# Optimization experiments

Measured on AMD Instinct MI355X. Metric: run time of the kernel, lower is better.

The kernel has to match this reference:

```python
import jax, jax.numpy as jnp
import numpy as np

B, S, D = 2, 2048, 2048
H = 16
HD = D // H
FF = 8192
EPS = 1e-5


def _layer_norm(x, g, b):
    mu = jnp.mean(x, axis=-1, keepdims=True)
    var = jnp.mean(jnp.square(x - mu), axis=-1, keepdims=True)
    return (x - mu) * jax.lax.rsqrt(var + EPS) * g + b


def setup_inputs() -> dict:
    key = jax.random.key(0)
    ks = jax.random.split(key, 8)
    s = 0.02
    return {
        "x": jax.random.normal(ks[0], (B, S, D), dtype=jnp.float32),
        "ln1_g": jnp.ones((D,), jnp.float32),
        "ln1_b": jnp.zeros((D,), jnp.float32),
        "qkv_w": jax.random.normal(ks[1], (D, 3 * D), dtype=jnp.float32) * s,
        "qkv_b": jnp.zeros((3 * D,), jnp.float32),
        "out_w": jax.random.normal(ks[2], (D, D), dtype=jnp.float32) * s,
        "out_b": jnp.zeros((D,), jnp.float32),
        "ln2_g": jnp.ones((D,), jnp.float32),
        "ln2_b": jnp.zeros((D,), jnp.float32),
        "w1": jax.random.normal(ks[3], (D, FF), dtype=jnp.float32) * s,
        "b1": jnp.zeros((FF,), jnp.float32),
        "w2": jax.random.normal(ks[4], (FF, D), dtype=jnp.float32) * s,
        "b2": jnp.zeros((D,), jnp.float32),
    }


def reference(x, ln1_g, ln1_b, qkv_w, qkv_b, out_w, out_b, ln2_g, ln2_b, w1, b1, w2, b2):
    # --- attention sub-block (pre-norm) ---
    residual = x
    h = _layer_norm(x, ln1_g, ln1_b)
    qkv = h @ qkv_w + qkv_b                      # [B,S,3D]
    q, k, v = jnp.split(qkv, 3, axis=-1)
    # [B,S,D] -> [B,H,S,HD]
    q = q.reshape(B, S, H, HD).transpose(0, 2, 1, 3)
    k = k.reshape(B, S, H, HD).transpose(0, 2, 1, 3)
    v = v.reshape(B, S, H, HD).transpose(0, 2, 1, 3)
    scores = jnp.einsum("bhqd,bhkd->bhqk", q, k)  # [B,H,S,S]
    causal = jnp.triu(jnp.ones((S, S), dtype=bool), k=1)
    scores = jnp.where(causal[None, None], -jnp.inf, scores)
    attn = jax.nn.softmax(scores / np.sqrt(HD).astype(np.float32), axis=-1)
    av = jnp.einsum("bhqk,bhkd->bhqd", attn, v)   # [B,H,S,HD]
    av = av.transpose(0, 2, 1, 3).reshape(B, S, D)
    x = residual + (av @ out_w + out_b)
    # --- FFN sub-block (pre-norm) ---
    residual = x
    h = _layer_norm(x, ln2_g, ln2_b)
    h = jax.nn.gelu(h @ w1 + b1, approximate=False)
    x = residual + (h @ w2 + b2)
    return x
```

## Files before the change

### kernel.cpp

```cpp
#include <hip/hip_runtime.h>
#include <hip/hip_bf16.h>

#define B_  2
#define S_  2048
#define D_  2048
#define H_  16
#define HD_ 128
#define FF_ 8192

typedef __bf16 bf16x8 __attribute__((ext_vector_type(8)));
typedef float  f32x4  __attribute__((ext_vector_type(4)));
typedef unsigned short u16;
typedef u16 u16x8 __attribute__((ext_vector_type(8)));

__device__ __forceinline__ u16 f2bf(float f) {
    union { float f; unsigned u; } c; c.f = f;
    unsigned u = c.u;
    u += 0x7fffu + ((u >> 16) & 1u);
    return (u16)(u >> 16);
}

__device__ __forceinline__ void gld16(void* lds, const void* g) {
    __builtin_amdgcn_global_load_lds(
        (const __attribute__((address_space(1))) unsigned int*)g,
        (__attribute__((address_space(3))) unsigned int*)lds,
        16, 0, 0);
}

__global__ __launch_bounds__(256)
void ln_kernel(const float* __restrict__ x, const float* __restrict__ g,
               const float* __restrict__ bb, u16* __restrict__ out)
{
    int row = blockIdx.x, tid = threadIdx.x;
    const float4* xr = (const float4*)(x + (size_t)row * D_);
    float4 a = xr[tid], c = xr[tid + 256];
    float s  = a.x + a.y + a.z + a.w + c.x + c.y + c.z + c.w;
    float s2 = a.x*a.x + a.y*a.y + a.z*a.z + a.w*a.w
             + c.x*c.x + c.y*c.y + c.z*c.z + c.w*c.w;
    #pragma unroll
    for (int off = 32; off > 0; off >>= 1) {
        s  += __shfl_down(s,  off, 64);
        s2 += __shfl_down(s2, off, 64);
    }
    __shared__ float red[16];
    __shared__ float mr[2];
    int wid = tid >> 6, lane = tid & 63;
    if (lane == 0) { red[wid] = s; red[8 + wid] = s2; }
    __syncthreads();
    if (tid == 0) {
        float ts = red[0] + red[1] + red[2] + red[3];
        float t2 = red[8] + red[9] + red[10] + red[11];
        float mu = ts * (1.0f / D_);
        float var = t2 * (1.0f / D_) - mu * mu;
        mr[0] = mu; mr[1] = rsqrtf(var + 1e-5f);
    }
    __syncthreads();
    float mu = mr[0], rstd = mr[1];
    const float4* gg = (const float4*)g;
    const float4* bv = (const float4*)bb;
    float4 g0 = gg[tid], g1 = gg[tid + 256];
    float4 b0 = bv[tid], b1 = bv[tid + 256];
    u16* orow = out + (size_t)row * D_;
    ushort4 o0, o1;
    o0.x = f2bf((a.x - mu) * rstd * g0.x + b0.x);
    o0.y = f2bf((a.y - mu) * rstd * g0.y + b0.y);
    o0.z = f2bf((a.z - mu) * rstd * g0.z + b0.z);
    o0.w = f2bf((a.w - mu) * rstd * g0.w + b0.w);
    o1.x = f2bf((c.x - mu) * rstd * g1.x + b1.x);
    o1.y = f2bf((c.y - mu) * rstd * g1.y + b1.y);
    o1.z = f2bf((c.z - mu) * rstd * g1.z + b1.z);
    o1.w = f2bf((c.w - mu) * rstd * g1.w + b1.w);
    *(ushort4*)&orow[tid * 4]         = o0;
    *(ushort4*)&orow[(tid + 256) * 4] = o1;
}

__global__ __launch_bounds__(256)
void tcvt_kernel(const float* __restrict__ W, u16* __restrict__ WT, int K, int N)
{
    __shared__ float t[32][33];
    int n0 = blockIdx.x << 5, k0 = blockIdx.y << 5;
    int tx = threadIdx.x & 31, ty = threadIdx.x >> 5;
    #pragma unroll
    for (int i = 0; i < 32; i += 8)
        t[ty + i][tx] = W[(size_t)(k0 + ty + i) * N + n0 + tx];
    __syncthreads();
    #pragma unroll
    for (int i = 0; i < 32; i += 8)
        WT[(size_t)(n0 + ty + i) * K + k0 + tx] = f2bf(t[tx][ty + i]);
}

template<int EPI>
__global__ __launch_bounds__(256)
void gemm_kernel(const u16* __restrict__ A, const u16* __restrict__ BT,
                 const float* __restrict__ bias, const float* __restrict__ res,
                 void* __restrict__ outv, int M, int N, int K)
{
    __shared__ u16 ldsA[128 * 32];
    __shared__ u16 ldsB[128 * 32];
    int tid = threadIdx.x;
    int wid = tid >> 6, lane = tid & 63;
    int wm = wid >> 1, wn = wid & 1;
    int quad = lane >> 4, l16 = lane & 15;
    int m0 = blockIdx.y << 7, n0 = blockIdx.x << 7;

    f32x4 acc[4][4] = {};

    const u16* gA0 = A  + (size_t)(m0 + wid * 32 + (lane >> 2)) * K + ((lane & 3) << 3);
    const u16* gA1 = gA0 + (size_t)16 * K;
    const u16* gB0 = BT + (size_t)(n0 + wid * 32 + (lane >> 2)) * K + ((lane & 3) << 3);
    const u16* gB1 = gB0 + (size_t)16 * K;
    u16* lA0 = ldsA + wid * 1024;
    u16* lA1 = ldsA + wid * 1024 + 512;
    u16* lB0 = ldsB + wid * 1024;
    u16* lB1 = ldsB + wid * 1024 + 512;

    for (int k0 = 0; k0 < K; k0 += 32) {
        gld16(lA0, gA0 + k0);
        gld16(lA1, gA1 + k0);
        gld16(lB0, gB0 + k0);
        gld16(lB1, gB1 + k0);
        __syncthreads();
        bf16x8 af[4], bf[4];
        #pragma unroll
        for (int t = 0; t < 4; t++) {
            af[t] = *(const bf16x8*)&ldsA[(wm * 64 + t * 16 + l16) * 32 + quad * 8];
            bf[t] = *(const bf16x8*)&ldsB[(wn * 64 + t * 16 + l16) * 32 + quad * 8];
        }
        #pragma unroll
        for (int i = 0; i < 4; i++)
            #pragma unroll
            for (int j = 0; j < 4; j++)
                acc[i][j] = __builtin_amdgcn_mfma_f32_16x16x32_bf16(af[i], bf[j], acc[i][j], 0, 0, 0);
        __syncthreads();
    }

    u16*   outb = (u16*)outv;
    float* outf = (float*)outv;
    int colb = n0 + wn * 64, rowb = m0 + wm * 64;
    #pragma unroll
    for (int j = 0; j < 4; j++) {
        int col = colb + j * 16 + l16;
        float bv = bias[col];
        #pragma unroll
        for (int i = 0; i < 4; i++) {
            int row0 = rowb + i * 16 + (quad << 2);
            #pragma unroll
            for (int r = 0; r < 4; r++) {
                float v = acc[i][j][r] + bv;
                size_t idx = (size_t)(row0 + r) * N + col;
                if (EPI == 2) {
                    outf[idx] = v + res[idx];
                } else {
                    if (EPI == 1) v = 0.5f * v * (1.0f + erff(v * 0.70710678118654752f));
                    outb[idx] = f2bf(v);
                }
            }
        }
    }
}

__global__ __launch_bounds__(256, 2)
void attn_kernel(const u16* __restrict__ qkv, u16* __restrict__ av)
{
    __shared__ u16 ldsK[4][64][32];
    __shared__ unsigned ldsVT[128][36];
    __shared__ u16 ldsP[4][32][72];
    int tid = threadIdx.x, wid = tid >> 6, lane = tid & 63;
    int quad = lane >> 4, l16 = lane & 15;
    int bh = blockIdx.y, b = bh >> 4, h = bh & 15;
    int qx = gridDim.x - 1 - blockIdx.x;
    int q0 = qx << 7;
    const u16* base = qkv + (size_t)b * S_ * (3 * D_);

    bf16x8 aq[2][4];
    #pragma unroll
    for (int set = 0; set < 2; set++) {
        int qrow = q0 + set * 64 + wid * 16 + l16;
        const u16* qp = base + (size_t)qrow * (3 * D_) + h * HD_;
        #pragma unroll
        for (int kk = 0; kk < 4; kk++)
            aq[set][kk] = *(const bf16x8*)(qp + kk * 32 + quad * 8);
    }

    float m_i[2][4], l_i[2][4];
    f32x4 oacc[2][8] = {};
    #pragma unroll
    for (int s = 0; s < 2; s++)
        #pragma unroll
        for (int r = 0; r < 4; r++) { m_i[s][r] = -1e30f; l_i[s][r] = 0.f; }

    const float scale = 0.088388347648318447f;
    int ntile = 2 * qx + 2;
    for (int jt = 0; jt < ntile; jt++) {
        int j0 = jt << 6;
        #pragma unroll
        for (int j = 0; j < 4; j++) {
            int c = wid * 4 + j;
            int kk = c >> 2, kb = c & 3;
            int key = (kb << 4) + (lane >> 2);
            const u16* g = base + (size_t)(j0 + key) * (3 * D_) + D_ + h * HD_
                         + kk * 32 + ((lane & 3) << 3);
            gld16((u16*)ldsK + c * 512, g);
        }
        {
            int kp = lane & 31, dhalf = lane >> 5;
            #pragma unroll
            for (int p = 0; p < 2; p++) {
                int doff = wid * 32 + p * 16 + dhalf * 8;
                const u16* g0 = base + (size_t)(j0 + 2 * kp) * (3 * D_)
                              + 2 * D_ + h * HD_ + doff;
                u16x8 v0 = *(const u16x8*)g0;
                u16x8 v1 = *(const u16x8*)(g0 + 3 * D_);
                #pragma unroll
                for (int k = 0; k < 8; k++)
                    ldsVT[doff + k][kp] = (unsigned)v0[k] | ((unsigned)v1[k] << 16);
            }
        }
        __syncthreads();
        f32x4 sacc[2][4] = {};
        #pragma unroll
        for (int kk = 0; kk < 4; kk++)
            #pragma unroll
            for (int n = 0; n < 4; n++) {
                bf16x8 bfr = *(const bf16x8*)&ldsK[kk][(n << 4) + l16][quad << 3];
                sacc[0][n] = __builtin_amdgcn_mfma_f32_16x16x32_bf16(aq[0][kk], bfr, sacc[0][n], 0, 0, 0);
                sacc[1][n] = __builtin_amdgcn_mfma_f32_16x16x32_bf16(aq[1][kk], bfr, sacc[1][n], 0, 0, 0);
            }
        #pragma unroll
        for (int set = 0; set < 2; set++) {
            float rowmax[4] = {-1e30f, -1e30f, -1e30f, -1e30f};
            #pragma unroll
            for (int n = 0; n < 4; n++) {
                int key = j0 + (n << 4) + l16;
                #pragma unroll
                for (int r = 0; r < 4; r++) {
                    float xv = sacc[set][n][r] * scale;
                    int qr = q0 + set * 64 + wid * 16 + (quad << 2) + r;
                    if (key > qr) xv = -1e30f;
                    sacc[set][n][r] = xv;
                    rowmax[r] = fmaxf(rowmax[r], xv);
                }
            }
            #pragma unroll
            for (int off = 1; off < 16; off <<= 1)
                #pragma unroll
                for (int r = 0; r < 4; r++)
                    rowmax[r] = fmaxf(rowmax[r], __shfl_xor(rowmax[r], off, 64));
            float alpha[4], rsum[4];
            #pragma unroll
            for (int r = 0; r < 4; r++) {
                float mn = fmaxf(m_i[set][r], rowmax[r]);
                alpha[r] = __expf(m_i[set][r] - mn);
                m_i[set][r] = mn;
                rsum[r] = 0.f;
            }
            #pragma unroll
            for (int n = 0; n < 4; n++)
                #pragma unroll
                for (int r = 0; r < 4; r++) {
                    float p = __expf(sacc[set][n][r] - m_i[set][r]);
                    rsum[r] += p;
                    ldsP[wid][set * 16 + (quad << 2) + r][(n << 4) + l16] = f2bf(p);
                }
            #pragma unroll
            for (int off = 1; off < 16; off <<= 1)
                #pragma unroll
                for (int r = 0; r < 4; r++)
                    rsum[r] += __shfl_xor(rsum[r], off, 64);
            #pragma unroll
            for (int r = 0; r < 4; r++)
                l_i[set][r] = l_i[set][r] * alpha[r] + rsum[r];
            #pragma unroll
            for (int n = 0; n < 8; n++)
                #pragma unroll
                for (int r = 0; r < 4; r++)
                    oacc[set][n][r] *= alpha[r];
        }
        #pragma unroll
        for (int ks = 0; ks < 2; ks++) {
            bf16x8 pa0 = *(const bf16x8*)&ldsP[wid][l16]     [(ks << 5) + (quad << 3)];
            bf16x8 pa1 = *(const bf16x8*)&ldsP[wid][16 + l16][(ks << 5) + (quad << 3)];
            #pragma unroll
            for (int n = 0; n < 8; n++) {
                bf16x8 vb = *(const bf16x8*)&ldsVT[(n << 4) + l16][(ks << 4) + (quad << 2)];
                oacc[0][n] = __builtin_amdgcn_mfma_f32_16x16x32_bf16(pa0, vb, oacc[0][n], 0, 0, 0);
                oacc[1][n] = __builtin_amdgcn_mfma_f32_16x16x32_bf16(pa1, vb, oacc[1][n], 0, 0, 0);
            }
        }
        __syncthreads();
    }
    #pragma unroll
    for (int set = 0; set < 2; set++)
        #pragma unroll
        for (int r = 0; r < 4; r++) {
            float inv = 1.0f / l_i[set][r];
            int qr = q0 + set * 64 + wid * 16 + (quad << 2) + r;
            u16* op = av + (size_t)(b * S_ + qr) * D_ + h * HD_;
            #pragma unroll
            for (int n = 0; n < 8; n++)
                op[(n << 4) + l16] = f2bf(oacc[set][n][r] * inv);
        }
}

extern "C" void kernel_launch(void* const* d_in, const int* in_sizes, int n_in,
                              void* d_out, int out_size, void* d_ws, size_t ws_size,
                              hipStream_t stream)
{
    const float* x     = (const float*)d_in[0];
    const float* ln1_g = (const float*)d_in[1];
    const float* ln1_b = (const float*)d_in[2];
    const float* qkv_w = (const float*)d_in[3];
    const float* qkv_b = (const float*)d_in[4];
    const float* out_w = (const float*)d_in[5];
    const float* out_b = (const float*)d_in[6];
    const float* ln2_g = (const float*)d_in[7];
    const float* ln2_b = (const float*)d_in[8];
    const float* w1    = (const float*)d_in[9];
    const float* b1    = (const float*)d_in[10];
    const float* w2    = (const float*)d_in[11];
    const float* b2    = (const float*)d_in[12];
    float* out = (float*)d_out;

    char* ws  = (char*)d_ws;
    u16* wT   = (u16*)ws;
    u16* hbuf = (u16*)(ws + (32u << 20));
    u16* big  = (u16*)(ws + (48u << 20));
    u16* qkvb = big;
    u16* ffb  = big;

    dim3 blk(256);

    ln_kernel<<<dim3(B_ * S_), blk, 0, stream>>>(x, ln1_g, ln1_b, hbuf);
    tcvt_kernel<<<dim3(6144 / 32, 2048 / 32), blk, 0, stream>>>(qkv_w, wT, 2048, 6144);
    gemm_kernel<0><<<dim3(6144 / 128, 4096 / 128), blk, 0, stream>>>(
        hbuf, wT, qkv_b, nullptr, (void*)qkvb, 4096, 6144, 2048);
    attn_kernel<<<dim3(S_ / 128, B_ * H_), blk, 0, stream>>>(qkvb, hbuf);
    tcvt_kernel<<<dim3(2048 / 32, 2048 / 32), blk, 0, stream>>>(out_w, wT, 2048, 2048);
    gemm_kernel<2><<<dim3(2048 / 128, 4096 / 128), blk, 0, stream>>>(
        hbuf, wT, out_b, x, (void*)out, 4096, 2048, 2048);
    ln_kernel<<<dim3(B_ * S_), blk, 0, stream>>>(out, ln2_g, ln2_b, hbuf);
    tcvt_kernel<<<dim3(8192 / 32, 2048 / 32), blk, 0, stream>>>(w1, wT, 2048, 8192);
    gemm_kernel<1><<<dim3(8192 / 128, 4096 / 128), blk, 0, stream>>>(
        hbuf, wT, b1, nullptr, (void*)ffb, 4096, 8192, 2048);
    tcvt_kernel<<<dim3(2048 / 32, 8192 / 32), blk, 0, stream>>>(w2, wT, 8192, 2048);
    gemm_kernel<2><<<dim3(2048 / 128, 4096 / 128), blk, 0, stream>>>(
        ffb, wT, b2, out, (void*)out, 4096, 2048, 8192);
}
```

Before: 1.025 ms.

## Double GEMM K-tile to 64 with XOR-swizzled LDS and banded block order

The GEMM kernel now stages 64-wide K slices per iteration instead of 32, which halves the number of barrier pairs per tile. Global-to-LDS loads use an XOR swizzle on the 16-byte column chunk to avoid LDS bank conflicts on the fragment reads. Blocks are launched on a 1D grid and remapped so that groups of 16 N-tiles sweep all M-tiles, aiming for better L2 reuse of the weight panels. LDS use doubles to 32 KB per block, which may lower occupancy.

```diff
diff --git a/kernel.cpp b/kernel.cpp
--- a/kernel.cpp
+++ b/kernel.cpp
@@ -95,42 +95,56 @@
                  const float* __restrict__ bias, const float* __restrict__ res,
                  void* __restrict__ outv, int M, int N, int K)
 {
-    __shared__ u16 ldsA[128 * 32];
-    __shared__ u16 ldsB[128 * 32];
+    __shared__ u16 ldsA[128 * 64];
+    __shared__ u16 ldsB[128 * 64];
     int tid = threadIdx.x;
     int wid = tid >> 6, lane = tid & 63;
     int wm = wid >> 1, wn = wid & 1;
     int quad = lane >> 4, l16 = lane & 15;
-    int m0 = blockIdx.y << 7, n0 = blockIdx.x << 7;
+
+    int tiles_m = M >> 7;
+    int bandsz = tiles_m << 4;
+    int lin = blockIdx.x;
+    int band = lin / bandsz, rr = lin % bandsz;
+    int m0 = (rr >> 4) << 7;
+    int n0 = ((band << 4) + (rr & 15)) << 7;
 
     f32x4 acc[4][4] = {};
 
-    const u16* gA0 = A  + (size_t)(m0 + wid * 32 + (lane >> 2)) * K + ((lane & 3) << 3);
-    const u16* gA1 = gA0 + (size_t)16 * K;
-    const u16* gB0 = BT + (size_t)(n0 + wid * 32 + (lane >> 2)) * K + ((lane & 3) << 3);
-    const u16* gB1 = gB0 + (size_t)16 * K;
-    u16* lA0 = ldsA + wid * 1024;
-    u16* lA1 = ldsA + wid * 1024 + 512;
-    u16* lB0 = ldsB + wid * 1024;
-    u16* lB1 = ldsB + wid * 1024 + 512;
-
-    for (int k0 = 0; k0 < K; k0 += 32) {
-        gld16(lA0, gA0 + k0);
-        gld16(lA1, gA1 + k0);
-        gld16(lB0, gB0 + k0);
-        gld16(lB1, gB1 + k0);
+    int r8 = lane >> 3, c8 = lane & 7;
+    int gc = (c8 ^ (r8 & 7)) << 3;
+    const u16* pA = A  + (size_t)(m0 + wid * 32 + r8) * K + gc;
+    const u16* pB = BT + (size_t)(n0 + wid * 32 + r8) * K + gc;
+    u16* lA = ldsA + wid * 32 * 64;
+    u16* lB = ldsB + wid * 32 * 64;
+    int sw = l16 & 7;
+
+    for (int k0 = 0; k0 < K; k0 += 64) {
+        #pragma unroll
+        for (int j = 0; j < 4; j++) {
+            gld16(lA + j * 512, pA + (size_t)j * 8 * K + k0);
+            gld16(lB + j * 512, pB + (size_t)j * 8 * K + k0);
+        }
         __syncthreads();
-        bf16x8 af[4], bf[4];
-        #pragma unroll
-        for (int t = 0; t < 4; t++) {
-            af[t] = *(const bf16x8*)&ldsA[(wm * 64 + t * 16 + l16) * 32 + quad * 8];
-            bf[t] = *(const bf16x8*)&ldsB[(wn * 64 + t * 16 + l16) * 32 + quad * 8];
-        }
-        #pragma unroll
-        for (int i = 0; i < 4; i++)
-            #pragma unroll
-            for (int j = 0; j < 4; j++)
-                acc[i][j] = __builtin_amdgcn_mfma_f32_16x16x32_bf16(af[i], bf[j], acc[i][j], 0, 0, 0);
+        #pragma unroll
+        for (int kk = 0; kk < 2; kk++) {
+            bf16x8 af[4], bf[4];
+            int co0 = ((kk * 4 + 0) ^ sw) << 3;
+            int co1 = ((kk * 4 + 1) ^ sw) << 3;
+            int co2 = ((kk * 4 + 2) ^ sw) << 3;
+            int co3 = ((kk * 4 + 3) ^ sw) << 3;
+            int co = quad == 0 ? co0 : quad == 1 ? co1 : quad == 2 ? co2 : co3;
+            #pragma unroll
+            for (int t = 0; t < 4; t++) {
+                af[t] = *(const bf16x8*)&ldsA[(wm * 64 + t * 16 + l16) * 64 + co];
+                bf[t] = *(const bf16x8*)&ldsB[(wn * 64 + t * 16 + l16) * 64 + co];
+            }
+            #pragma unroll
+            for (int i = 0; i < 4; i++)
+                #pragma unroll
+                for (int j = 0; j < 4; j++)
+                    acc[i][j] = __builtin_amdgcn_mfma_f32_16x16x32_bf16(af[i], bf[j], acc[i][j], 0, 0, 0);
+        }
         __syncthreads();
     }
 
@@ -332,17 +346,17 @@
 
     ln_kernel<<<dim3(B_ * S_), blk, 0, stream>>>(x, ln1_g, ln1_b, hbuf);
     tcvt_kernel<<<dim3(6144 / 32, 2048 / 32), blk, 0, stream>>>(qkv_w, wT, 2048, 6144);
-    gemm_kernel<0><<<dim3(6144 / 128, 4096 / 128), blk, 0, stream>>>(
+    gemm_kernel<0><<<dim3((6144 / 128) * (4096 / 128)), blk, 0, stream>>>(
         hbuf, wT, qkv_b, nullptr, (void*)qkvb, 4096, 6144, 2048);
     attn_kernel<<<dim3(S_ / 128, B_ * H_), blk, 0, stream>>>(qkvb, hbuf);
     tcvt_kernel<<<dim3(2048 / 32, 2048 / 32), blk, 0, stream>>>(out_w, wT, 2048, 2048);
-    gemm_kernel<2><<<dim3(2048 / 128, 4096 / 128), blk, 0, stream>>>(
+    gemm_kernel<2><<<dim3((2048 / 128) * (4096 / 128)), blk, 0, stream>>>(
         hbuf, wT, out_b, x, (void*)out, 4096, 2048, 2048);
     ln_kernel<<<dim3(B_ * S_), blk, 0, stream>>>(out, ln2_g, ln2_b, hbuf);
     tcvt_kernel<<<dim3(8192 / 32, 2048 / 32), blk, 0, stream>>>(w1, wT, 2048, 8192);
-    gemm_kernel<1><<<dim3(8192 / 128, 4096 / 128), blk, 0, stream>>>(
+    gemm_kernel<1><<<dim3((8192 / 128) * (4096 / 128)), blk, 0, stream>>>(
         hbuf, wT, b1, nullptr, (void*)ffb, 4096, 8192, 2048);
     tcvt_kernel<<<dim3(2048 / 32, 8192 / 32), blk, 0, stream>>>(w2, wT, 8192, 2048);
-    gemm_kernel<2><<<dim3(2048 / 128, 4096 / 128), blk, 0, stream>>>(
+    gemm_kernel<2><<<dim3((2048 / 128) * (4096 / 128)), blk, 0, stream>>>(
         ffb, wT, b2, out, (void*)out, 4096, 2048, 8192);
 }
```

After: 951.7 us. -7.1%, faster.
